# Performance work log

Measured on AMD Instinct MI355X. Metric: run time of the kernel, lower is better.

The kernel has to match this reference:

```python
import jax, jax.numpy as jnp
import numpy as np

B, N, D = 4, 1024, 1024   # batch, seq (x and context must match), model dim
H, DH = 16, 64            # heads, dim_head; inner_dim = H*DH = 1024
INNER = H * DH
EPS = 1e-5


def setup_inputs() -> dict:
    key = jax.random.key(0)
    ks = jax.random.split(key, 12)
    s = 0.02
    return {
        "x": jax.random.normal(ks[0], (B, N, D), dtype=jnp.float32),
        "context": jax.random.normal(ks[1], (B, N, D), dtype=jnp.float32),
        # weights stored as [in, out] (torch Linear weight transposed)
        "W_qk": jax.random.normal(ks[2], (D, INNER), dtype=jnp.float32) * s,
        "W_cqk": jax.random.normal(ks[3], (D, INNER), dtype=jnp.float32) * s,
        "W_v": jax.random.normal(ks[4], (D, INNER), dtype=jnp.float32) * s,
        "W_cv": jax.random.normal(ks[5], (D, INNER), dtype=jnp.float32) * s,
        "W_out": jax.random.normal(ks[6], (INNER, D), dtype=jnp.float32) * s,
        "b_out": jax.random.normal(ks[7], (D,), dtype=jnp.float32) * s,
        "W_cout": jax.random.normal(ks[8], (INNER, D), dtype=jnp.float32) * s,
        "b_cout": jax.random.normal(ks[9], (D,), dtype=jnp.float32) * s,
        "gamma": jnp.ones((D,), dtype=jnp.float32),
        "beta": jnp.zeros((D,), dtype=jnp.float32),
    }


def _split_heads(t):  # [b, n, h*d] -> [b, h, n, d]
    b, n, _ = t.shape
    return t.reshape(b, n, H, DH).transpose(0, 2, 1, 3)


def _merge_heads(t):  # [b, h, n, d] -> [b, n, h*d]
    b, h, n, d = t.shape
    return t.transpose(0, 2, 1, 3).reshape(b, n, h * d)


def _layernorm(y, gamma, beta):
    mu = jnp.mean(y, axis=-1, keepdims=True)
    var = jnp.var(y, axis=-1, keepdims=True)
    return gamma * (y - mu) * jax.lax.rsqrt(var + EPS) + beta


def reference(x, context, W_qk, W_cqk, W_v, W_cv, W_out, b_out, W_cout, b_cout, gamma, beta):
    scale = DH ** -0.5
    res = x + context                       # residual (requires identical shapes)
    # prenorm=False -> identity norms; dropout=0; talking_heads=False -> identity
    qk = _split_heads(x @ W_qk)             # [b,h,i,d]
    v = _split_heads(x @ W_v)               # [b,h,i,d]
    cqk = _split_heads(context @ W_cqk)     # [b,h,j,d]
    cv = _split_heads(context @ W_cv)       # [b,h,j,d]

    sim = jnp.einsum('bhid,bhjd->bhij', qk, cqk) * scale  # shared similarity
    attn = jax.nn.softmax(sim, axis=-1)      # row softmax (x attends to context)
    context_attn = jax.nn.softmax(sim, axis=-2)  # column softmax (context attends to x)

    out = jnp.einsum('bhij,bhjd->bhid', attn, cv)          # [b,h,i,d]
    context_out = jnp.einsum('bhji,bhjd->bhid', context_attn, v)  # [b,h,i,d]

    out = _merge_heads(out) @ W_out + b_out
    context_out = _merge_heads(context_out) @ W_cout + b_cout
    return _layernorm(out + context_out, gamma, beta) + res
```

## Files before the change

### kernel.cpp

```cpp
#include <hip/hip_runtime.h>
#include <hip/hip_bf16.h>

typedef unsigned short u16;
typedef __bf16 bf16x8 __attribute__((ext_vector_type(8)));
typedef float   f32x4 __attribute__((ext_vector_type(4)));
typedef u16     u16x8 __attribute__((ext_vector_type(8)));
typedef u16     u16x4 __attribute__((ext_vector_type(4)));

#define DEV static __device__ __forceinline__

DEV float bf2f(u16 b) { unsigned int u = ((unsigned int)b) << 16; return __builtin_bit_cast(float, u); }
DEV u16   f2bf(float f) { return __builtin_bit_cast(u16, (__bf16)f); }
DEV bf16x8 ldb(const u16* p) { return __builtin_bit_cast(bf16x8, *(const u16x8*)p); }

DEV f32x4 mfma_bf16(bf16x8 a, bf16x8 b, f32x4 c) {
  return __builtin_amdgcn_mfma_f32_16x16x32_bf16(a, b, c, 0, 0, 0);
}

#define LDA 40

__global__ __launch_bounds__(256) void detect_dtype(const u16* x, int* flag) {
  int tid = threadIdx.x;
  u16 lo = x[tid * 2];
  float v = bf2f(lo);
  float av = fabsf(v);
  bool plaus = (av > 1e-4f && av < 50.f);
  __shared__ int cnt;
  if (tid == 0) cnt = 0;
  __syncthreads();
  if (plaus) atomicAdd(&cnt, 1);
  __syncthreads();
  if (tid == 0) *flag = (cnt >= 128) ? 1 : 0;
}

struct Cv2 { const void* s[2]; u16* d[2]; };
__global__ __launch_bounds__(256) void convert_big(Cv2 p, const int* flagp) {
  int fl = *flagp;
  const void* src = p.s[blockIdx.z];
  u16* dst = p.d[blockIdx.z];
  size_t i = ((size_t)blockIdx.x * 256 + threadIdx.x) * 8;
  if (fl) {
    *(u16x8*)(dst + i) = *(const u16x8*)((const u16*)src + i);
  } else {
    const float* s = (const float*)src + i;
    u16x8 o;
#pragma unroll
    for (int k = 0; k < 8; ++k) o[k] = f2bf(s[k]);
    *(u16x8*)(dst + i) = o;
  }
}

struct Sm4 { const void* s[4]; u16* d[4]; };
__global__ __launch_bounds__(256) void convert_smalls(Sm4 p, const int* flagp) {
  int fl = *flagp;
  const void* src = p.s[blockIdx.x];
  u16* dst = p.d[blockIdx.x];
  int i = threadIdx.x * 4;
#pragma unroll
  for (int k = 0; k < 4; ++k)
    dst[i + k] = fl ? ((const u16*)src)[i + k] : f2bf(((const float*)src)[i + k]);
}

struct T6 { const void* s[6]; u16* d[6]; };

__global__ __launch_bounds__(256) void transpose6(T6 t, const int* flagp) {
  int fl = *flagp;
  __shared__ u16 tile[32][33];
  const void* src = t.s[blockIdx.z];
  u16* dst = t.d[blockIdx.z];
  int x0 = blockIdx.x * 32, y0 = blockIdx.y * 32;
  int tx = threadIdx.x & 31, ty = threadIdx.x >> 5;
#pragma unroll
  for (int i = 0; i < 32; i += 8) {
    size_t idx = (size_t)(y0 + ty + i) * 1024 + x0 + tx;
    tile[ty + i][tx] = fl ? ((const u16*)src)[idx] : f2bf(((const float*)src)[idx]);
  }
  __syncthreads();
#pragma unroll
  for (int i = 0; i < 32; i += 8)
    dst[(size_t)(x0 + ty + i) * 1024 + y0 + tx] = tile[tx][ty + i];
}

struct Proj4 { const u16* A[4]; const u16* Bt[4]; u16* C[4]; int mode[4]; };

__global__ __launch_bounds__(256) void gemm_proj(Proj4 p) {
  const int K = 1024, Nn = 1024;
  const u16* A  = p.A[blockIdx.z];
  const u16* Bt = p.Bt[blockIdx.z];
  u16* C = p.C[blockIdx.z];
  int mode = p.mode[blockIdx.z];

  __shared__ __align__(16) u16 As[128 * LDA];
  __shared__ __align__(16) u16 Bs[128 * LDA];

  int tid = threadIdx.x, lane = tid & 63, w = tid >> 6;
  int wm = w & 1, wn = w >> 1;
  int q4 = lane >> 4, c = lane & 15;
  int m0 = blockIdx.y * 128, n0 = blockIdx.x * 128;

  int ar = 32 * w + (lane >> 2);
  int ag = (lane & 3) * 8;
  int sa = ar * LDA + ag;

  const u16* pA = A  + (size_t)(m0 + ar) * K + ag;
  const u16* pB = Bt + (size_t)(n0 + ar) * K + ag;

  u16x8 a0 = *(const u16x8*)(pA);
  u16x8 a1 = *(const u16x8*)(pA + (size_t)16 * K);
  u16x8 b0 = *(const u16x8*)(pB);
  u16x8 b1 = *(const u16x8*)(pB + (size_t)16 * K);

  f32x4 acc[4][4] = {};

  for (int k0 = 0; k0 < K; k0 += 32) {
    __syncthreads();
    *(u16x8*)(As + sa)            = a0;
    *(u16x8*)(As + sa + 16 * LDA) = a1;
    *(u16x8*)(Bs + sa)            = b0;
    *(u16x8*)(Bs + sa + 16 * LDA) = b1;
    __syncthreads();
    if (k0 + 32 < K) {
      a0 = *(const u16x8*)(pA + k0 + 32);
      a1 = *(const u16x8*)(pA + (size_t)16 * K + k0 + 32);
      b0 = *(const u16x8*)(pB + k0 + 32);
      b1 = *(const u16x8*)(pB + (size_t)16 * K + k0 + 32);
    }
    bf16x8 af[4], bfr[4];
#pragma unroll
    for (int i = 0; i < 4; ++i) af[i]  = ldb(As + (wm * 64 + i * 16 + c) * LDA + q4 * 8);
#pragma unroll
    for (int j = 0; j < 4; ++j) bfr[j] = ldb(Bs + (wn * 64 + j * 16 + c) * LDA + q4 * 8);
#pragma unroll
    for (int i = 0; i < 4; ++i)
#pragma unroll
      for (int j = 0; j < 4; ++j)
        acc[i][j] = mfma_bf16(af[i], bfr[j], acc[i][j]);
  }

  if (mode == 0) {
#pragma unroll
    for (int i = 0; i < 4; ++i) {
      int mrow = m0 + wm * 64 + i * 16 + q4 * 4;
#pragma unroll
      for (int j = 0; j < 4; ++j) {
        int col = n0 + wn * 64 + j * 16 + c;
#pragma unroll
        for (int r = 0; r < 4; ++r)
          C[(size_t)(mrow + r) * Nn + col] = f2bf(acc[i][j][r]);
      }
    }
  } else {
    int bidx = m0 >> 10;
#pragma unroll
    for (int i = 0; i < 4; ++i) {
      int mrow = m0 + wm * 64 + i * 16 + q4 * 4;
      int jj = mrow & 1023;
#pragma unroll
      for (int j = 0; j < 4; ++j) {
        int col = n0 + wn * 64 + j * 16 + c;
        int h = col >> 6, dh = col & 63;
        u16x4 pk;
#pragma unroll
        for (int r = 0; r < 4; ++r) pk[r] = f2bf(acc[i][j][r]);
        *(u16x4*)(C + ((size_t)((bidx * 16 + h) * 64 + dh)) * 1024 + jj) = pk;
      }
    }
  }
}

__global__ __launch_bounds__(256) void flash_attn(const u16* Q, const u16* Kg,
                                                  const u16* Vt, u16* O) {
  int bh = blockIdx.y; int b = bh >> 4, h = bh & 15;
  int i0 = blockIdx.x * 64;
  int tid = threadIdx.x, lane = tid & 63, w = tid >> 6;
  int q4 = lane >> 4, c = lane & 15;

  __shared__ __align__(16) u16 Ks[64 * 72];
  __shared__ __align__(16) u16 Vs[64 * 72];
  __shared__ __align__(16) u16 Ps[4][16 * 72];

  const size_t qoff = ((size_t)(b * 1024 + i0 + w * 16 + c)) * 1024 + h * 64 + q4 * 8;
  bf16x8 qf0 = ldb(Q + qoff);
  bf16x8 qf1 = ldb(Q + qoff + 32);

  f32x4 of[4] = {};
  f32x4 lacc = {};
  bf16x8 ones;
#pragma unroll
  for (int k = 0; k < 8; ++k) ones[k] = (__bf16)1.0f;

  int jr = tid >> 2, seg = (tid & 3) * 16;
  const u16* krow_base = Kg + ((size_t)(b * 1024 + jr)) * 1024 + h * 64 + seg;
  const u16* vrow_base = Vt + ((size_t)((b * 16 + h) * 64 + jr)) * 1024 + seg;
  const float scale = 0.125f;

  for (int j0 = 0; j0 < 1024; j0 += 64) {
    const u16* ks = krow_base + (size_t)j0 * 1024;
    u16x8 kv0 = *(const u16x8*)(ks);
    u16x8 kv1 = *(const u16x8*)(ks + 8);
    const u16* vs = vrow_base + j0;
    u16x8 vv0 = *(const u16x8*)(vs);
    u16x8 vv1 = *(const u16x8*)(vs + 8);
    __syncthreads();
    *(u16x8*)(Ks + jr * 72 + seg)     = kv0;
    *(u16x8*)(Ks + jr * 72 + seg + 8) = kv1;
    *(u16x8*)(Vs + jr * 72 + seg)     = vv0;
    *(u16x8*)(Vs + jr * 72 + seg + 8) = vv1;
    __syncthreads();

    f32x4 sf[4] = {};
#pragma unroll
    for (int jc = 0; jc < 4; ++jc) {
      bf16x8 k0f = ldb(Ks + (jc * 16 + c) * 72 + q4 * 8);
      bf16x8 k1f = ldb(Ks + (jc * 16 + c) * 72 + 32 + q4 * 8);
      sf[jc] = mfma_bf16(k0f, qf0, sf[jc]);
      sf[jc] = mfma_bf16(k1f, qf1, sf[jc]);
    }

#pragma unroll
    for (int jc = 0; jc < 4; ++jc) {
      u16x4 pk;
#pragma unroll
      for (int r = 0; r < 4; ++r) {
        float s = fminf(fmaxf(sf[jc][r] * scale, -60.f), 60.f);
        pk[r] = f2bf(__expf(s));
      }
      *(u16x4*)(Ps[w] + c * 72 + jc * 16 + q4 * 4) = pk;
    }

    asm volatile("s_waitcnt lgkmcnt(0)" ::: "memory");

    bf16x8 pf0 = ldb(Ps[w] + c * 72 + q4 * 8);
    bf16x8 pf1 = ldb(Ps[w] + c * 72 + 32 + q4 * 8);

    lacc = mfma_bf16(pf0, ones, lacc);
    lacc = mfma_bf16(pf1, ones, lacc);

#pragma unroll
    for (int dc = 0; dc < 4; ++dc) {
      bf16x8 v0f = ldb(Vs + (dc * 16 + c) * 72 + q4 * 8);
      bf16x8 v1f = ldb(Vs + (dc * 16 + c) * 72 + 32 + q4 * 8);
      of[dc] = mfma_bf16(pf0, v0f, of[dc]);
      of[dc] = mfma_bf16(pf1, v1f, of[dc]);
    }
  }

  float inv[4];
#pragma unroll
  for (int r = 0; r < 4; ++r) inv[r] = 1.0f / lacc[r];
#pragma unroll
  for (int dc = 0; dc < 4; ++dc) {
    int col = h * 64 + dc * 16 + c;
#pragma unroll
    for (int r = 0; r < 4; ++r) {
      int irow = i0 + w * 16 + q4 * 4 + r;
      O[((size_t)(b * 1024 + irow)) * 1024 + col] = f2bf(of[dc][r] * inv[r]);
    }
  }
}

__global__ __launch_bounds__(256) void gemm_final(const u16* A1, const u16* B1t,
                                                  const u16* A2, const u16* B2t,
                                                  const u16* b1, const u16* b2,
                                                  float* Y) {
  const int K = 1024, Nn = 1024;
  __shared__ __align__(16) u16 As[128 * LDA];
  __shared__ __align__(16) u16 Bs[128 * LDA];

  int tid = threadIdx.x, lane = tid & 63, w = tid >> 6;
  int wm = w & 1, wn = w >> 1;
  int q4 = lane >> 4, c = lane & 15;
  int m0 = blockIdx.y * 128, n0 = blockIdx.x * 128;

  int ar = 32 * w + (lane >> 2);
  int ag = (lane & 3) * 8;
  int sa = ar * LDA + ag;

  const u16* A1b = A1 + (size_t)(m0 + ar) * K + ag;
  const u16* A2b = A2 + (size_t)(m0 + ar) * K + ag;
  const u16* B1b = B1t + (size_t)(n0 + ar) * K + ag;
  const u16* B2b = B2t + (size_t)(n0 + ar) * K + ag;

  u16x8 a0 = *(const u16x8*)(A1b);
  u16x8 a1 = *(const u16x8*)(A1b + (size_t)16 * K);
  u16x8 b0 = *(const u16x8*)(B1b);
  u16x8 b1v = *(const u16x8*)(B1b + (size_t)16 * K);

  f32x4 acc[4][4] = {};

  for (int kk = 0; kk < 64; ++kk) {
    __syncthreads();
    *(u16x8*)(As + sa)            = a0;
    *(u16x8*)(As + sa + 16 * LDA) = a1;
    *(u16x8*)(Bs + sa)            = b0;
    *(u16x8*)(Bs + sa + 16 * LDA) = b1v;
    __syncthreads();
    if (kk + 1 < 64) {
      const u16* An = (kk + 1 < 32) ? A1b : A2b;
      const u16* Bn = (kk + 1 < 32) ? B1b : B2b;
      int k0n = ((kk + 1) & 31) * 32;
      a0  = *(const u16x8*)(An + k0n);
      a1  = *(const u16x8*)(An + (size_t)16 * K + k0n);
      b0  = *(const u16x8*)(Bn + k0n);
      b1v = *(const u16x8*)(Bn + (size_t)16 * K + k0n);
    }
    bf16x8 af[4], bfr[4];
#pragma unroll
    for (int i = 0; i < 4; ++i) af[i]  = ldb(As + (wm * 64 + i * 16 + c) * LDA + q4 * 8);
#pragma unroll
    for (int j = 0; j < 4; ++j) bfr[j] = ldb(Bs + (wn * 64 + j * 16 + c) * LDA + q4 * 8);
#pragma unroll
    for (int i = 0; i < 4; ++i)
#pragma unroll
      for (int j = 0; j < 4; ++j)
        acc[i][j] = mfma_bf16(af[i], bfr[j], acc[i][j]);
  }

#pragma unroll
  for (int i = 0; i < 4; ++i) {
    int mrow = m0 + wm * 64 + i * 16 + q4 * 4;
#pragma unroll
    for (int j = 0; j < 4; ++j) {
      int col = n0 + wn * 64 + j * 16 + c;
      float bias = bf2f(b1[col]) + bf2f(b2[col]);
#pragma unroll
      for (int r = 0; r < 4; ++r)
        Y[(size_t)(mrow + r) * Nn + col] = acc[i][j][r] + bias;
    }
  }
}

__global__ __launch_bounds__(256) void ln_res(const float* Y, const u16* gamma, const u16* beta,
                                              const u16* x, const u16* ctx, void* out,
                                              const int* flagp) {
  int fl = *flagp;
  int row = blockIdx.x;
  int tid = threadIdx.x;
  const float* y = Y + (size_t)row * 1024;
  float4 v = *(const float4*)(y + tid * 4);
  float s  = v.x + v.y + v.z + v.w;
  float s2 = v.x * v.x + v.y * v.y + v.z * v.z + v.w * v.w;
#pragma unroll
  for (int off = 1; off < 64; off <<= 1) { s += __shfl_xor(s, off); s2 += __shfl_xor(s2, off); }
  __shared__ float red[8];
  int w = tid >> 6, lane = tid & 63;
  if (lane == 0) { red[w] = s; red[w + 4] = s2; }
  __syncthreads();
  float S  = red[0] + red[1] + red[2] + red[3];
  float S2 = red[4] + red[5] + red[6] + red[7];
  float mu  = S * (1.0f / 1024.0f);
  float var = S2 * (1.0f / 1024.0f) - mu * mu;
  float rs = rsqrtf(var + 1e-5f);
  size_t base = (size_t)row * 1024 + tid * 4;
  u16x4 gv = *(const u16x4*)(gamma + tid * 4);
  u16x4 bv = *(const u16x4*)(beta + tid * 4);
  u16x4 xv = *(const u16x4*)(x + base);
  u16x4 cv = *(const u16x4*)(ctx + base);
  float vv[4] = {v.x, v.y, v.z, v.w};
  float o[4];
#pragma unroll
  for (int k = 0; k < 4; ++k)
    o[k] = bf2f(gv[k]) * (vv[k] - mu) * rs + bf2f(bv[k]) + bf2f(xv[k]) + bf2f(cv[k]);
  if (fl) {
    u16x4 ov;
#pragma unroll
    for (int k = 0; k < 4; ++k) ov[k] = f2bf(o[k]);
    *(u16x4*)((u16*)out + base) = ov;
  } else {
    *(float4*)((float*)out + base) = make_float4(o[0], o[1], o[2], o[3]);
  }
}

__global__ __launch_bounds__(256) void sentinel(u16* out) {
  size_t i = ((size_t)blockIdx.x * 256 + threadIdx.x) * 8;
  u16 v = f2bf(12345.0f);
  u16x8 o = {v, v, v, v, v, v, v, v};
  *(u16x8*)(out + i) = o;
}

extern "C" void kernel_launch(void* const* d_in, const int* in_sizes, int n_in,
                              void* d_out, int out_size, void* d_ws, size_t ws_size,
                              hipStream_t stream) {
  (void)in_sizes; (void)n_in; (void)out_size;
  const size_t MB = 1024 * 1024;
  const size_t NEED = 61 * MB;
  if (ws_size < NEED) {
    sentinel<<<2048, 256, 0, stream>>>((u16*)d_out);
    return;
  }

  char* ws = (char*)d_ws;
  u16* wt[6];
  for (int i = 0; i < 6; ++i) wt[i] = (u16*)(ws + (size_t)i * 2 * MB);
  u16* xc   = (u16*)(ws + 12 * MB);
  u16* cc   = (u16*)(ws + 20 * MB);
  u16* qk   = (u16*)(ws + 28 * MB);
  u16* cqk  = (u16*)(ws + 36 * MB);
  u16* vt   = (u16*)(ws + 44 * MB);
  u16* cvt  = (u16*)(ws + 52 * MB);
  u16* oa   = (u16*)(ws + 0);
  u16* ca   = (u16*)(ws + 52 * MB);
  float* y  = (float*)(ws + 28 * MB);
  int* flag = (int*)(ws + 60 * MB);
  u16* b1c  = (u16*)(ws + 60 * MB + 4096);
  u16* b2c  = (u16*)(ws + 60 * MB + 8192);
  u16* gc   = (u16*)(ws + 60 * MB + 12288);
  u16* bc   = (u16*)(ws + 60 * MB + 16384);

  detect_dtype<<<1, 256, 0, stream>>>((const u16*)d_in[0], flag);

  Cv2 cv;
  cv.s[0] = d_in[0]; cv.d[0] = xc;
  cv.s[1] = d_in[1]; cv.d[1] = cc;
  convert_big<<<dim3(2048, 1, 2), 256, 0, stream>>>(cv, flag);

  Sm4 sm;
  sm.s[0] = d_in[7]; sm.d[0] = b1c;
  sm.s[1] = d_in[9]; sm.d[1] = b2c;
  sm.s[2] = d_in[10]; sm.d[2] = gc;
  sm.s[3] = d_in[11]; sm.d[3] = bc;
  convert_smalls<<<4, 256, 0, stream>>>(sm, flag);

  T6 t;
  t.s[0] = d_in[2]; t.d[0] = wt[0];
  t.s[1] = d_in[3]; t.d[1] = wt[1];
  t.s[2] = d_in[4]; t.d[2] = wt[2];
  t.s[3] = d_in[5]; t.d[3] = wt[3];
  t.s[4] = d_in[6]; t.d[4] = wt[4];
  t.s[5] = d_in[8]; t.d[5] = wt[5];
  transpose6<<<dim3(32, 32, 6), 256, 0, stream>>>(t, flag);

  Proj4 p;
  p.A[0] = xc; p.Bt[0] = wt[0]; p.C[0] = qk;  p.mode[0] = 0;
  p.A[1] = cc; p.Bt[1] = wt[1]; p.C[1] = cqk; p.mode[1] = 0;
  p.A[2] = xc; p.Bt[2] = wt[2]; p.C[2] = vt;  p.mode[2] = 1;
  p.A[3] = cc; p.Bt[3] = wt[3]; p.C[3] = cvt; p.mode[3] = 1;
  gemm_proj<<<dim3(8, 32, 4), 256, 0, stream>>>(p);

  flash_attn<<<dim3(16, 64), 256, 0, stream>>>(qk, cqk, cvt, oa);
  flash_attn<<<dim3(16, 64), 256, 0, stream>>>(cqk, qk, vt, ca);

  gemm_final<<<dim3(8, 32), 256, 0, stream>>>(oa, wt[4], ca, wt[5], b1c, b2c, y);

  ln_res<<<4096, 256, 0, stream>>>(y, gc, bc, xc, cc, d_out, flag);
}
```

Before: 293.2 us.

## Load GEMM tiles directly into LDS with XOR swizzle and grouped block order

Both projection and final GEMMs now copy global tiles straight into shared memory with global_load_lds, replacing register staging and the padded LDS layout. An XOR swizzle on the 16-byte column chunks avoids bank conflicts without padding, and block indices are remapped so consecutive blocks share the same N tile for better L2 reuse. The register prefetch of the next tile is gone, so each iteration waits on vmcnt(0) right after issuing loads, which exposes global latency unless occupancy hides it.

```diff
diff --git a/kernel.cpp b/kernel.cpp
--- a/kernel.cpp
+++ b/kernel.cpp
@@ -17,7 +17,11 @@
   return __builtin_amdgcn_mfma_f32_16x16x32_bf16(a, b, c, 0, 0, 0);
 }
 
-#define LDA 40
+DEV void gl16(const u16* g, u16* l) {
+  __builtin_amdgcn_global_load_lds((const __attribute__((address_space(1))) unsigned int*)g,
+                                   (__attribute__((address_space(3))) unsigned int*)l,
+                                   16, 0, 0);
+}
 
 __global__ __launch_bounds__(256) void detect_dtype(const u16* x, int* flag) {
   int tid = threadIdx.x;
@@ -90,46 +94,40 @@
   u16* C = p.C[blockIdx.z];
   int mode = p.mode[blockIdx.z];
 
-  __shared__ __align__(16) u16 As[128 * LDA];
-  __shared__ __align__(16) u16 Bs[128 * LDA];
+  __shared__ __align__(16) u16 As[128 * 32];
+  __shared__ __align__(16) u16 Bs[128 * 32];
 
   int tid = threadIdx.x, lane = tid & 63, w = tid >> 6;
   int wm = w & 1, wn = w >> 1;
   int q4 = lane >> 4, c = lane & 15;
-  int m0 = blockIdx.y * 128, n0 = blockIdx.x * 128;
-
-  int ar = 32 * w + (lane >> 2);
-  int ag = (lane & 3) * 8;
-  int sa = ar * LDA + ag;
-
-  const u16* pA = A  + (size_t)(m0 + ar) * K + ag;
-  const u16* pB = Bt + (size_t)(n0 + ar) * K + ag;
-
-  u16x8 a0 = *(const u16x8*)(pA);
-  u16x8 a1 = *(const u16x8*)(pA + (size_t)16 * K);
-  u16x8 b0 = *(const u16x8*)(pB);
-  u16x8 b1 = *(const u16x8*)(pB + (size_t)16 * K);
+
+  int bid = blockIdx.y * 8 + blockIdx.x;
+  int wg  = (bid & 7) * 32 + (bid >> 3);
+  int m0 = (wg >> 3) * 128, n0 = (wg & 7) * 128;
+
+  int r0 = w * 32 + (lane >> 2);
+  int cc = (lane & 3) ^ ((lane >> 3) & 3);
+  const u16* pA0 = A  + (size_t)(m0 + r0) * K + cc * 8;
+  const u16* pB0 = Bt + (size_t)(n0 + r0) * K + cc * 8;
+  u16* lA0 = As + w * 1024;
+  u16* lB0 = Bs + w * 1024;
+  int qs = (q4 ^ ((c >> 1) & 3)) * 8;
 
   f32x4 acc[4][4] = {};
 
   for (int k0 = 0; k0 < K; k0 += 32) {
     __syncthreads();
-    *(u16x8*)(As + sa)            = a0;
-    *(u16x8*)(As + sa + 16 * LDA) = a1;
-    *(u16x8*)(Bs + sa)            = b0;
-    *(u16x8*)(Bs + sa + 16 * LDA) = b1;
-    __syncthreads();
-    if (k0 + 32 < K) {
-      a0 = *(const u16x8*)(pA + k0 + 32);
-      a1 = *(const u16x8*)(pA + (size_t)16 * K + k0 + 32);
-      b0 = *(const u16x8*)(pB + k0 + 32);
-      b1 = *(const u16x8*)(pB + (size_t)16 * K + k0 + 32);
-    }
+    gl16(pA0 + k0,                  lA0);
+    gl16(pA0 + (size_t)16 * K + k0, lA0 + 512);
+    gl16(pB0 + k0,                  lB0);
+    gl16(pB0 + (size_t)16 * K + k0, lB0 + 512);
+    asm volatile("s_waitcnt vmcnt(0)" ::: "memory");
+    __syncthreads();
     bf16x8 af[4], bfr[4];
 #pragma unroll
-    for (int i = 0; i < 4; ++i) af[i]  = ldb(As + (wm * 64 + i * 16 + c) * LDA + q4 * 8);
-#pragma unroll
-    for (int j = 0; j < 4; ++j) bfr[j] = ldb(Bs + (wn * 64 + j * 16 + c) * LDA + q4 * 8);
+    for (int i = 0; i < 4; ++i) af[i]  = ldb(As + (wm * 64 + i * 16 + c) * 32 + qs);
+#pragma unroll
+    for (int j = 0; j < 4; ++j) bfr[j] = ldb(Bs + (wn * 64 + j * 16 + c) * 32 + qs);
 #pragma unroll
     for (int i = 0; i < 4; ++i)
 #pragma unroll
@@ -264,51 +262,45 @@
                                                   const u16* b1, const u16* b2,
                                                   float* Y) {
   const int K = 1024, Nn = 1024;
-  __shared__ __align__(16) u16 As[128 * LDA];
-  __shared__ __align__(16) u16 Bs[128 * LDA];
+  __shared__ __align__(16) u16 As[128 * 32];
+  __shared__ __align__(16) u16 Bs[128 * 32];
 
   int tid = threadIdx.x, lane = tid & 63, w = tid >> 6;
   int wm = w & 1, wn = w >> 1;
   int q4 = lane >> 4, c = lane & 15;
-  int m0 = blockIdx.y * 128, n0 = blockIdx.x * 128;
-
-  int ar = 32 * w + (lane >> 2);
-  int ag = (lane & 3) * 8;
-  int sa = ar * LDA + ag;
-
-  const u16* A1b = A1 + (size_t)(m0 + ar) * K + ag;
-  const u16* A2b = A2 + (size_t)(m0 + ar) * K + ag;
-  const u16* B1b = B1t + (size_t)(n0 + ar) * K + ag;
-  const u16* B2b = B2t + (size_t)(n0 + ar) * K + ag;
-
-  u16x8 a0 = *(const u16x8*)(A1b);
-  u16x8 a1 = *(const u16x8*)(A1b + (size_t)16 * K);
-  u16x8 b0 = *(const u16x8*)(B1b);
-  u16x8 b1v = *(const u16x8*)(B1b + (size_t)16 * K);
+
+  int bid = blockIdx.y * 8 + blockIdx.x;
+  int wg  = (bid & 7) * 32 + (bid >> 3);
+  int m0 = (wg >> 3) * 128, n0 = (wg & 7) * 128;
+
+  int r0 = w * 32 + (lane >> 2);
+  int cc = (lane & 3) ^ ((lane >> 3) & 3);
+  const u16* A1p = A1  + (size_t)(m0 + r0) * K + cc * 8;
+  const u16* A2p = A2  + (size_t)(m0 + r0) * K + cc * 8;
+  const u16* B1p = B1t + (size_t)(n0 + r0) * K + cc * 8;
+  const u16* B2p = B2t + (size_t)(n0 + r0) * K + cc * 8;
+  u16* lA0 = As + w * 1024;
+  u16* lB0 = Bs + w * 1024;
+  int qs = (q4 ^ ((c >> 1) & 3)) * 8;
 
   f32x4 acc[4][4] = {};
 
   for (int kk = 0; kk < 64; ++kk) {
-    __syncthreads();
-    *(u16x8*)(As + sa)            = a0;
-    *(u16x8*)(As + sa + 16 * LDA) = a1;
-    *(u16x8*)(Bs + sa)            = b0;
-    *(u16x8*)(Bs + sa + 16 * LDA) = b1v;
-    __syncthreads();
-    if (kk + 1 < 64) {
-      const u16* An = (kk + 1 < 32) ? A1b : A2b;
-      const u16* Bn = (kk + 1 < 32) ? B1b : B2b;
-      int k0n = ((kk + 1) & 31) * 32;
-      a0  = *(const u16x8*)(An + k0n);
-      a1  = *(const u16x8*)(An + (size_t)16 * K + k0n);
-      b0  = *(const u16x8*)(Bn + k0n);
-      b1v = *(const u16x8*)(Bn + (size_t)16 * K + k0n);
-    }
+    const u16* Ap = (kk < 32) ? A1p : A2p;
+    const u16* Bp = (kk < 32) ? B1p : B2p;
+    int k0 = (kk & 31) * 32;
+    __syncthreads();
+    gl16(Ap + k0,                  lA0);
+    gl16(Ap + (size_t)16 * K + k0, lA0 + 512);
+    gl16(Bp + k0,                  lB0);
+    gl16(Bp + (size_t)16 * K + k0, lB0 + 512);
+    asm volatile("s_waitcnt vmcnt(0)" ::: "memory");
+    __syncthreads();
     bf16x8 af[4], bfr[4];
 #pragma unroll
-    for (int i = 0; i < 4; ++i) af[i]  = ldb(As + (wm * 64 + i * 16 + c) * LDA + q4 * 8);
-#pragma unroll
-    for (int j = 0; j < 4; ++j) bfr[j] = ldb(Bs + (wn * 64 + j * 16 + c) * LDA + q4 * 8);
+    for (int i = 0; i < 4; ++i) af[i]  = ldb(As + (wm * 64 + i * 16 + c) * 32 + qs);
+#pragma unroll
+    for (int j = 0; j < 4; ++j) bfr[j] = ldb(Bs + (wn * 64 + j * 16 + c) * 32 + qs);
 #pragma unroll
     for (int i = 0; i < 4; ++i)
 #pragma unroll
```

Measured after the change: 292.8 us. Within noise of the previous version (-0.2%).
